# Optimization experiments

Hardware: AMD Instinct MI355X
Metric: run time of the kernel (lower is better)

Reference implementation:

```python
import jax, jax.numpy as jnp
import numpy as np


def setup_inputs() -> dict:
    key = jax.random.key(0)
    k1, k2 = jax.random.split(key)
    B, Fin, N = 8, 64, 4096
    Fout, K = 64, 20
    x = jax.random.normal(k1, (B, Fin, N), dtype=jnp.float32)
    W = jax.random.normal(k2, (Fout, 2 * Fin), dtype=jnp.float32) * (1.0 / np.sqrt(2 * Fin))
    b = jnp.zeros((Fout,), dtype=jnp.float32)
    return {"x": x, "W": W, "b": b, "k": K}


def reference(x, W, b, k):
    # x: [B, Fin, N]; W: [Fout, 2Fin] (1x1 conv weight); b: [Fout]
    B, Fin, N = x.shape
    xt = jnp.swapaxes(x, 1, 2)                      # [B, N, Fin]
    sq = jnp.sum(xt * xt, axis=2)                   # [B, N]
    # pairwise squared distances: ||xi||^2 - 2 xi.xj + ||xj||^2
    dist = -2.0 * jnp.einsum('bnf,bmf->bnm', xt, xt) + sq[:, :, None] + sq[:, None, :]
    # ascending sort, drop self (index 0), keep k nearest neighbors
    idx = jnp.argsort(dist, axis=2)[:, :, 1:k + 1]  # [B, N, k] int
    # gather neighbor features per batch
    nbr = jax.vmap(lambda pts, i: pts[i])(xt, idx)  # [B, N, k, Fin]
    central = xt[:, :, None, :]                     # [B, N, 1, Fin]
    ee = jnp.concatenate(
        [jnp.broadcast_to(central, (B, N, k, Fin)), nbr - central], axis=-1
    )                                               # [B, N, k, 2Fin]
    # 1x1 conv == dense over channel dim, then bias, then max over k
    h = jnp.einsum('bnkf,of->bnko', ee, W) + b      # [B, N, k, Fout]
    out = jnp.max(h, axis=2)                        # [B, N, Fout]
    return jnp.swapaxes(out, 1, 2)                  # [B, Fout, N]
```

## Files before the change

### kernel.cpp

```cpp
#include <hip/hip_runtime.h>
#include <hip/hip_bf16.h>
#include <float.h>


#define BB 8
#define FF 64
#define NN 4096
#define KK 20
#define CAP 60
#define SS 2
#define PAD 0.3f

typedef unsigned short ushort_t;
typedef unsigned long long u64;
typedef __attribute__((ext_vector_type(8))) _Float16 half8;
typedef __attribute__((ext_vector_type(4))) float floatx4;
typedef __attribute__((ext_vector_type(2))) float floatx2;
typedef __attribute__((ext_vector_type(2))) unsigned short ushortx2;
typedef __attribute__((ext_vector_type(4))) unsigned int uintx4;

__device__ __forceinline__ size_t plidx16(int b, int n, int k) {
  return ((size_t)b * 256 + (n >> 4)) * 1024 + (size_t)(k >> 3) * 128 + (size_t)(n & 15) * 8 + (k & 7);
}

__global__ void __launch_bounds__(256) prep_kernel(
    const float* __restrict__ x, const float* __restrict__ W,
    float* __restrict__ sq, float* __restrict__ Q,
    ushort_t* __restrict__ ph, ushort_t* __restrict__ pm)
{
  __shared__ float xs[64][65];
  __shared__ float w2[64][65];
  int t = threadIdx.x;
  int b = blockIdx.x >> 6;
  int n0 = (blockIdx.x & 63) << 6;
  const float* xb = x + (size_t)b * FF * NN;

  int nl = t & 63, fq = t >> 6;
  #pragma unroll
  for (int i = 0; i < 16; ++i) {
    int f = fq + i * 4;
    xs[f][nl] = xb[(size_t)f * NN + n0 + nl];
  }
  #pragma unroll
  for (int i = 0; i < 16; ++i) {
    int id = i * 256 + t;
    int o = id >> 6, f = id & 63;
    w2[o][f] = W[o * 128 + 64 + f];
  }
  __syncthreads();

  if (t < 64) {
    float s = 0.f;
    #pragma unroll
    for (int f = 0; f < FF; ++f) { float v = xs[f][t]; s += v * v; }
    sq[b * NN + n0 + t] = s;
  }
  int o = t & 63, g = t >> 6;
  for (int i = 0; i < 16; ++i) {
    int r = g + i * 4;
    int n = n0 + r;
    float acc = 0.f;
    #pragma unroll
    for (int f = 0; f < FF; ++f) acc += w2[o][f] * xs[f][r];
    Q[((size_t)b * NN + n) * FF + o] = acc;

    float v = xs[o][r] * 1.41421356237309515f;
    _Float16 hh = (_Float16)v;
    float hf = (float)hh;
    _Float16 mm = (_Float16)((v - hf) * 4096.0f);
    size_t pb = plidx16(b, n, o);
    ph[pb] = __builtin_bit_cast(unsigned short, hh);
    pm[pb] = __builtin_bit_cast(unsigned short, mm);
  }
}

__device__ __forceinline__ void bitonic32f(float& v0, float& v1, int l15)
{
  #pragma unroll
  for (int k = 2; k <= 32; k <<= 1) {
    #pragma unroll
    for (int j = k >> 1; j >= 1; j >>= 1) {
      bool dirup = ((2 * l15) & k) == 0;
      if (j >= 2) {
        int lj = j >> 1;
        float p0 = __shfl_xor(v0, lj, 16);
        float p1 = __shfl_xor(v1, lj, 16);
        bool lower = (l15 & lj) == 0;
        bool keepmin = (dirup == lower);
        v0 = keepmin ? fminf(v0, p0) : fmaxf(v0, p0);
        v1 = keepmin ? fminf(v1, p1) : fmaxf(v1, p1);
      } else {
        float lo = fminf(v0, v1), hi = fmaxf(v0, v1);
        v0 = dirup ? lo : hi;
        v1 = dirup ? hi : lo;
      }
    }
  }
}

__device__ __forceinline__ void bitonic64k(u64& v0, u64& v1, int l31)
{
  #pragma unroll
  for (int k = 2; k <= 64; k <<= 1) {
    #pragma unroll
    for (int j = k >> 1; j >= 1; j >>= 1) {
      bool dirup = ((2 * l31) & k) == 0;
      if (j >= 2) {
        int lj = j >> 1;
        u64 p0 = __shfl_xor(v0, lj, 32);
        u64 p1 = __shfl_xor(v1, lj, 32);
        bool lower = (l31 & lj) == 0;
        bool keepmin = (dirup == lower);
        u64 a0 = v0 < p0 ? v0 : p0, b0 = v0 < p0 ? p0 : v0;
        u64 a1 = v1 < p1 ? v1 : p1, b1 = v1 < p1 ? p1 : v1;
        v0 = keepmin ? a0 : b0;
        v1 = keepmin ? a1 : b1;
      } else {
        u64 lo = v0 < v1 ? v0 : v1, hi = v0 < v1 ? v1 : v0;
        v0 = dirup ? lo : hi;
        v1 = dirup ? hi : lo;
      }
    }
  }
}

__device__ __forceinline__ u64 mkkey(float d, unsigned short idx)
{
  unsigned ub = __float_as_uint(d);
  unsigned mono = ub ^ (0x80000000u | (unsigned)((int)ub >> 31));
  return ((u64)mono << 16) | idx;
}

__global__ void __launch_bounds__(256) knn_kernel(
    const ushort_t* __restrict__ ph, const ushort_t* __restrict__ pm,
    const float* __restrict__ sq, u64* __restrict__ keys2)
{
  __shared__ ushort_t stg[2][2][2048];
  __shared__ float    bufd[4][16][CAP];
  __shared__ ushort_t bufi[4][16][CAP];
  __shared__ int scnt[4][16];

  const int t = threadIdx.x;
  const int lane = t & 63;
  const int l15 = lane & 15;
  const int q = lane >> 4;
  const int wv = t >> 6;
  const int blk = blockIdx.x;
  const int b = blk & 7;
  const int k2 = blk >> 3;
  const int slice = k2 & 1;
  const int g = k2 >> 1;
  const int n0w = (g * 4 + wv) * 16;

  const float* __restrict__ sqb = sq + (size_t)b * NN;
  const float MS = 2.44140625e-4f;
  const int laneoff = q * 128 + l15 * 8;

  const bool hasdiag = ((n0w >> 11) == slice);
  const int dmc = (n0w & 2047) >> 5;

  half8 Ah[2], Am[2];
  {
    size_t abase = ((size_t)b * 256 + (n0w >> 4)) * 1024 + laneoff;
    #pragma unroll
    for (int s = 0; s < 2; ++s) {
      Ah[s] = *(const half8*)(ph + abase + s * 512);
      Am[s] = *(const half8*)(pm + abase + s * 512);
      uintx4 uh = __builtin_bit_cast(uintx4, Ah[s]); uh ^= 0x80008000u;
      uintx4 um = __builtin_bit_cast(uintx4, Am[s]); um ^= 0x80008000u;
      Ah[s] = __builtin_bit_cast(half8, uh);
      Am[s] = __builtin_bit_cast(half8, um);
    }
  }

  const size_t slb = (size_t)b * 262144 + (size_t)slice * 131072;
  const uintx4* gph = (const uintx4*)(ph + slb) + t;
  const uintx4* gpm = (const uintx4*)(pm + slb) + t;

  float m1[4], m2[4];
  #pragma unroll
  for (int r = 0; r < 4; ++r) { m1[r] = FLT_MAX; m2[r] = FLT_MAX; }

  {
    uintx4 v0s = gph[0];
    *((uintx4*)stg[0][0] + t) = v0s;
    __syncthreads();

    const float* psq = sqb + slice * 2048 + l15;
    for (int mc = 0; mc < 64; ++mc) {
      const int cur = mc & 1;
      uintx4 nx;
      if (mc < 63) nx = gph[(mc + 1) * 256];
      float sv0 = psq[0];
      float sv1 = psq[16];
      floatx4 a1[2];
      #pragma unroll
      for (int e = 0; e < 4; ++e) { a1[0][e] = sv0; a1[1][e] = sv1; }
      const ushort_t* sp = stg[cur][0] + laneoff;
      #pragma unroll
      for (int ti = 0; ti < 2; ++ti) {
        #pragma unroll
        for (int s = 0; s < 2; ++s) {
          half8 Bh = *(const half8*)(sp + ti * 1024 + s * 512);
          a1[ti] = __builtin_amdgcn_mfma_f32_16x16x32_f16(Ah[s], Bh, a1[ti], 0, 0, 0);
        }
      }
      if (hasdiag && mc == dmc) {
        const int m0 = slice * 2048 + mc * 32;
        #pragma unroll
        for (int ti = 0; ti < 2; ++ti) {
          int mcol = m0 + 16 * ti + l15;
          #pragma unroll
          for (int r = 0; r < 4; ++r)
            if (mcol == n0w + 4 * q + r) a1[ti][r] = FLT_MAX;
        }
      }
      #pragma unroll
      for (int r = 0; r < 4; ++r) {
        float c = fminf(a1[0][r], a1[1][r]);
        m2[r] = __builtin_amdgcn_fmed3f(c, m1[r], m2[r]);
        m1[r] = fminf(m1[r], c);
      }
      if (mc < 63) *((uintx4*)stg[cur ^ 1][0] + t) = nx;
      __syncthreads();
      psq += 32;
    }
  }

  float taupad[4];
  #pragma unroll
  for (int r = 0; r < 4; ++r) {
    float v0 = m1[r], v1 = m2[r];
    bitonic32f(v0, v1, l15);
    taupad[r] = __shfl(v1, 9, 16) + PAD;
  }

  int cnt[4];
  #pragma unroll
  for (int r = 0; r < 4; ++r) cnt[r] = 0;

  {
    uintx4 vh0 = gph[0];
    uintx4 vm0 = gpm[0];
    *((uintx4*)stg[0][0] + t) = vh0;
    *((uintx4*)stg[0][1] + t) = vm0;
    __syncthreads();

    const float* psq = sqb + slice * 2048 + l15;
    for (int mc = 0; mc < 64; ++mc) {
      const int cur = mc & 1;
      uintx4 nh, nm;
      if (mc < 63) { nh = gph[(mc + 1) * 256]; nm = gpm[(mc + 1) * 256]; }
      float sv0 = psq[0];
      float sv1 = psq[16];
      floatx4 a1[2], a2[2];
      #pragma unroll
      for (int e = 0; e < 4; ++e) {
        a1[0][e] = sv0; a1[1][e] = sv1;
        a2[0][e] = 0.f; a2[1][e] = 0.f;
      }
      const ushort_t* sp0 = stg[cur][0] + laneoff;
      const ushort_t* sp1 = stg[cur][1] + laneoff;
      #pragma unroll
      for (int ti = 0; ti < 2; ++ti) {
        #pragma unroll
        for (int s = 0; s < 2; ++s) {
          half8 Bh = *(const half8*)(sp0 + ti * 1024 + s * 512);
          half8 Bm = *(const half8*)(sp1 + ti * 1024 + s * 512);
          a1[ti] = __builtin_amdgcn_mfma_f32_16x16x32_f16(Ah[s], Bh, a1[ti], 0, 0, 0);
          a2[ti] = __builtin_amdgcn_mfma_f32_16x16x32_f16(Am[s], Bh, a2[ti], 0, 0, 0);
          a2[ti] = __builtin_amdgcn_mfma_f32_16x16x32_f16(Ah[s], Bm, a2[ti], 0, 0, 0);
        }
      }
      #pragma unroll
      for (int ti = 0; ti < 2; ++ti)
        #pragma unroll
        for (int r = 0; r < 4; ++r)
          a1[ti][r] = __builtin_fmaf(MS, a2[ti][r], a1[ti][r]);
      const int m0 = slice * 2048 + mc * 32;
      if (hasdiag && mc == dmc) {
        #pragma unroll
        for (int ti = 0; ti < 2; ++ti) {
          int mcol = m0 + 16 * ti + l15;
          #pragma unroll
          for (int r = 0; r < 4; ++r)
            if (mcol == n0w + 4 * q + r) a1[ti][r] = FLT_MAX;
        }
      }
      #pragma unroll
      for (int ti = 0; ti < 2; ++ti) {
        int mcol = m0 + 16 * ti + l15;
        #pragma unroll
        for (int r = 0; r < 4; ++r) {
          bool ok = a1[ti][r] <= taupad[r];
          unsigned long long bal = __ballot(ok);
          if (bal) {
            unsigned mh = (unsigned)((bal >> (q * 16)) & 0xFFFFull);
            int pre = __popc(mh & ((1u << l15) - 1u));
            int slot = cnt[r] + pre;
            if (ok && slot < CAP) {
              bufd[wv][4 * q + r][slot] = a1[ti][r];
              bufi[wv][4 * q + r][slot] = (ushort_t)mcol;
            }
            cnt[r] += __popc(mh);
          }
        }
      }
      if (mc < 63) {
        *((uintx4*)stg[cur ^ 1][0] + t) = nh;
        *((uintx4*)stg[cur ^ 1][1] + t) = nm;
      }
      __syncthreads();
      psq += 32;
    }
  }

  if (l15 == 0) {
    #pragma unroll
    for (int r = 0; r < 4; ++r) scnt[wv][4 * q + r] = cnt[r];
  }
  __builtin_amdgcn_s_waitcnt(0);

  const int l31 = t & 31;
  const int hfw = (t >> 5) & 1;
  #pragma unroll
  for (int i = 0; i < 8; ++i) {
    int rloc = hfw * 8 + i;
    int c = scnt[wv][rloc];
    c = c < CAP ? c : CAP;
    u64 k0 = ~0ull, k1 = ~0ull;
    if (2 * l31 < c) {
      floatx2  dv = *(const floatx2*)&bufd[wv][rloc][2 * l31];
      ushortx2 iv = *(const ushortx2*)&bufi[wv][rloc][2 * l31];
      k0 = mkkey(dv[0], iv[0]);
      if (2 * l31 + 1 < c) k1 = mkkey(dv[1], iv[1]);
    }
    bitonic64k(k0, k1, l31);
    u64 a = __shfl(k0, l31 >> 1, 32);
    u64 b2 = __shfl(k1, l31 >> 1, 32);
    u64 kv = (l31 & 1) ? b2 : a;
    if (l31 < KK) {
      size_t rowg = ((size_t)b * NN + n0w + rloc) * SS + slice;
      keys2[rowg * KK + l31] = kv;
    }
  }
}

__global__ void __launch_bounds__(256) merge_kernel(
    const u64* __restrict__ keys2, int* __restrict__ idxOut)
{
  int row = blockIdx.x * 256 + threadIdx.x;
  if (row >= BB * NN) return;
  u64 h[SS]; int p[SS];
  #pragma unroll
  for (int s = 0; s < SS; ++s) {
    p[s] = 0;
    h[s] = keys2[((size_t)row * SS + s) * KK];
  }
  int* op = idxOut + (size_t)row * KK;
  #pragma unroll
  for (int q = 0; q < KK; ++q) {
    int bs = 0;
    u64 bv = h[0];
    #pragma unroll
    for (int s = 1; s < SS; ++s) { if (h[s] < bv) { bv = h[s]; bs = s; } }
    op[q] = (int)(bv & 0xFFFFull);
    p[bs]++;
    h[bs] = (p[bs] < KK) ? keys2[((size_t)row * SS + bs) * KK + p[bs]] : ~0ull;
  }
}

__global__ void __launch_bounds__(256) gather_kernel(
    const float* __restrict__ x, const float* __restrict__ W,
    const float* __restrict__ bias,
    const float* __restrict__ Q, const int* __restrict__ idxIn,
    float* __restrict__ out)
{
  __shared__ float xs[64][65];
  __shared__ float wp[64][65];
  __shared__ float ot[64][65];
  __shared__ float bs[64];
  int t = threadIdx.x;
  int b = blockIdx.x >> 6;
  int n0 = (blockIdx.x & 63) << 6;
  const float* xb = x + (size_t)b * FF * NN;

  int nl0 = t & 63, fq = t >> 6;
  #pragma unroll
  for (int i = 0; i < 16; ++i) {
    int f = fq + i * 4;
    xs[f][nl0] = xb[(size_t)f * NN + n0 + nl0];
  }
  #pragma unroll
  for (int i = 0; i < 16; ++i) {
    int id = i * 256 + t;
    int o = id >> 6, f = id & 63;
    wp[o][f] = W[o * 128 + f] - W[o * 128 + 64 + f];
  }
  if (t < 64) bs[t] = bias[t];
  __syncthreads();

  int o = t & 63, g = t >> 6;
  for (int i = 0; i < 16; ++i) {
    int nl = g + i * 4;
    int n = n0 + nl;
    float p = bs[o];
    #pragma unroll
    for (int f = 0; f < FF; ++f) p += wp[o][f] * xs[f][nl];
    const int* ip = idxIn + ((size_t)b * NN + n) * KK;
    float m = -FLT_MAX;
    #pragma unroll
    for (int j = 0; j < KK; ++j) {
      int nb = ip[j];
      m = fmaxf(m, Q[((size_t)b * NN + nb) * FF + o]);
    }
    ot[nl][o] = p + m;
  }
  __syncthreads();
  for (int i = 0; i < 16; ++i) {
    int o2 = g + i * 4;
    int nl = t & 63;
    out[((size_t)b * FF + o2) * NN + n0 + nl] = ot[nl][o2];
  }
}

extern "C" void kernel_launch(void* const* d_in, const int* in_sizes, int n_in,
                              void* d_out, int out_size, void* d_ws, size_t ws_size,
                              hipStream_t stream)
{
  const float* x    = (const float*)d_in[0];
  const float* W    = (const float*)d_in[1];
  const float* bias = (const float*)d_in[2];
  float* out = (float*)d_out;

  int*   idxb = (int*)d_ws;
  float* sq   = (float*)(idxb + (size_t)BB * NN * KK);
  float* Q    = sq + (size_t)BB * NN;
  ushort_t* ph = (ushort_t*)(Q + (size_t)BB * NN * FF);
  ushort_t* pm = ph + (size_t)BB * NN * FF;
  u64*   keys2 = (u64*)(pm + (size_t)BB * NN * FF);

  prep_kernel<<<BB * (NN / 64), 256, 0, stream>>>(x, W, sq, Q, ph, pm);
  knn_kernel<<<BB * 64 * SS, 256, 0, stream>>>(ph, pm, sq, keys2);
  merge_kernel<<<(BB * NN + 255) / 256, 256, 0, stream>>>(keys2, idxb);
  gather_kernel<<<BB * (NN / 64), 256, 0, stream>>>(x, W, bias, Q, idxb, out);
}
```

Before: 256.8 us.

## Process 32 query rows per wave in kNN kernel to reuse B tiles

Each wave now computes distances for two 16-row query tiles instead of one. Every staged candidate fragment loaded from LDS therefore feeds twice as many MFMAs, and the knn grid is halved. This cuts LDS reads and global staging traffic per query. In exchange, registers per thread rise (twice the accumulators, thresholds and counters) and there are fewer blocks to spread across CUs. The candidate buffer cap is trimmed from 60 to 56 so the doubled LDS buffers fit.

```diff
diff --git a/kernel.cpp b/kernel.cpp
--- a/kernel.cpp
+++ b/kernel.cpp
@@ -7,7 +7,7 @@
 #define FF 64
 #define NN 4096
 #define KK 20
-#define CAP 60
+#define CAP 56
 #define SS 2
 #define PAD 0.3f
 
@@ -136,9 +136,9 @@
     const float* __restrict__ sq, u64* __restrict__ keys2)
 {
   __shared__ ushort_t stg[2][2][2048];
-  __shared__ float    bufd[4][16][CAP];
-  __shared__ ushort_t bufi[4][16][CAP];
-  __shared__ int scnt[4][16];
+  __shared__ float    bufd[4][32][CAP];
+  __shared__ ushort_t bufi[4][32][CAP];
+  __shared__ int scnt[4][32];
 
   const int t = threadIdx.x;
   const int lane = t & 63;
@@ -150,7 +150,7 @@
   const int k2 = blk >> 3;
   const int slice = k2 & 1;
   const int g = k2 >> 1;
-  const int n0w = (g * 4 + wv) * 16;
+  const int n0w = (g * 4 + wv) * 32;
 
   const float* __restrict__ sqb = sq + (size_t)b * NN;
   const float MS = 2.44140625e-4f;
@@ -159,17 +159,18 @@
   const bool hasdiag = ((n0w >> 11) == slice);
   const int dmc = (n0w & 2047) >> 5;
 
-  half8 Ah[2], Am[2];
-  {
-    size_t abase = ((size_t)b * 256 + (n0w >> 4)) * 1024 + laneoff;
+  half8 Ah[2][2], Am[2][2];
+  #pragma unroll
+  for (int w = 0; w < 2; ++w) {
+    size_t abase = ((size_t)b * 256 + (n0w >> 4) + w) * 1024 + laneoff;
     #pragma unroll
     for (int s = 0; s < 2; ++s) {
-      Ah[s] = *(const half8*)(ph + abase + s * 512);
-      Am[s] = *(const half8*)(pm + abase + s * 512);
-      uintx4 uh = __builtin_bit_cast(uintx4, Ah[s]); uh ^= 0x80008000u;
-      uintx4 um = __builtin_bit_cast(uintx4, Am[s]); um ^= 0x80008000u;
-      Ah[s] = __builtin_bit_cast(half8, uh);
-      Am[s] = __builtin_bit_cast(half8, um);
+      Ah[w][s] = *(const half8*)(ph + abase + s * 512);
+      Am[w][s] = *(const half8*)(pm + abase + s * 512);
+      uintx4 uh = __builtin_bit_cast(uintx4, Ah[w][s]); uh ^= 0x80008000u;
+      uintx4 um = __builtin_bit_cast(uintx4, Am[w][s]); um ^= 0x80008000u;
+      Ah[w][s] = __builtin_bit_cast(half8, uh);
+      Am[w][s] = __builtin_bit_cast(half8, um);
     }
   }
 
@@ -177,9 +178,9 @@
   const uintx4* gph = (const uintx4*)(ph + slb) + t;
   const uintx4* gpm = (const uintx4*)(pm + slb) + t;
 
-  float m1[4], m2[4];
-  #pragma unroll
-  for (int r = 0; r < 4; ++r) { m1[r] = FLT_MAX; m2[r] = FLT_MAX; }
+  float m1[8], m2[8];
+  #pragma unroll
+  for (int r = 0; r < 8; ++r) { m1[r] = FLT_MAX; m2[r] = FLT_MAX; }
 
   {
     uintx4 v0s = gph[0];
@@ -193,51 +194,60 @@
       if (mc < 63) nx = gph[(mc + 1) * 256];
       float sv0 = psq[0];
       float sv1 = psq[16];
-      floatx4 a1[2];
-      #pragma unroll
-      for (int e = 0; e < 4; ++e) { a1[0][e] = sv0; a1[1][e] = sv1; }
       const ushort_t* sp = stg[cur][0] + laneoff;
-      #pragma unroll
-      for (int ti = 0; ti < 2; ++ti) {
-        #pragma unroll
-        for (int s = 0; s < 2; ++s) {
-          half8 Bh = *(const half8*)(sp + ti * 1024 + s * 512);
-          a1[ti] = __builtin_amdgcn_mfma_f32_16x16x32_f16(Ah[s], Bh, a1[ti], 0, 0, 0);
-        }
+      half8 B00 = *(const half8*)(sp);
+      half8 B01 = *(const half8*)(sp + 512);
+      half8 B10 = *(const half8*)(sp + 1024);
+      half8 B11 = *(const half8*)(sp + 1536);
+      floatx4 a[2][2];
+      #pragma unroll
+      for (int w = 0; w < 2; ++w)
+        #pragma unroll
+        for (int e = 0; e < 4; ++e) { a[w][0][e] = sv0; a[w][1][e] = sv1; }
+      #pragma unroll
+      for (int w = 0; w < 2; ++w) {
+        a[w][0] = __builtin_amdgcn_mfma_f32_16x16x32_f16(Ah[w][0], B00, a[w][0], 0, 0, 0);
+        a[w][0] = __builtin_amdgcn_mfma_f32_16x16x32_f16(Ah[w][1], B01, a[w][0], 0, 0, 0);
+        a[w][1] = __builtin_amdgcn_mfma_f32_16x16x32_f16(Ah[w][0], B10, a[w][1], 0, 0, 0);
+        a[w][1] = __builtin_amdgcn_mfma_f32_16x16x32_f16(Ah[w][1], B11, a[w][1], 0, 0, 0);
       }
       if (hasdiag && mc == dmc) {
         const int m0 = slice * 2048 + mc * 32;
         #pragma unroll
-        for (int ti = 0; ti < 2; ++ti) {
-          int mcol = m0 + 16 * ti + l15;
+        for (int w = 0; w < 2; ++w)
           #pragma unroll
-          for (int r = 0; r < 4; ++r)
-            if (mcol == n0w + 4 * q + r) a1[ti][r] = FLT_MAX;
+          for (int ti = 0; ti < 2; ++ti) {
+            int mcol = m0 + 16 * ti + l15;
+            #pragma unroll
+            for (int r = 0; r < 4; ++r)
+              if (mcol == n0w + 16 * w + 4 * q + r) a[w][ti][r] = FLT_MAX;
+          }
+      }
+      #pragma unroll
+      for (int w = 0; w < 2; ++w)
+        #pragma unroll
+        for (int r = 0; r < 4; ++r) {
+          float c = fminf(a[w][0][r], a[w][1][r]);
+          m2[w * 4 + r] = __builtin_amdgcn_fmed3f(c, m1[w * 4 + r], m2[w * 4 + r]);
+          m1[w * 4 + r] = fminf(m1[w * 4 + r], c);
         }
-      }
-      #pragma unroll
-      for (int r = 0; r < 4; ++r) {
-        float c = fminf(a1[0][r], a1[1][r]);
-        m2[r] = __builtin_amdgcn_fmed3f(c, m1[r], m2[r]);
-        m1[r] = fminf(m1[r], c);
-      }
       if (mc < 63) *((uintx4*)stg[cur ^ 1][0] + t) = nx;
       __syncthreads();
       psq += 32;
     }
   }
 
-  float taupad[4];
-  #pragma unroll
-  for (int r = 0; r < 4; ++r) {
+  float taupad[8];
+  #pragma unroll
+  for (int r = 0; r < 8; ++r) {
     float v0 = m1[r], v1 = m2[r];
     bitonic32f(v0, v1, l15);
     taupad[r] = __shfl(v1, 9, 16) + PAD;
   }
 
-  int cnt[4];
-  #pragma unroll
-  for (int r = 0; r < 4; ++r) cnt[r] = 0;
+  int cnt[8];
+  #pragma unroll
+  for (int r = 0; r < 8; ++r) cnt[r] = 0;
 
   {
     uintx4 vh0 = gph[0];
@@ -253,59 +263,79 @@
       if (mc < 63) { nh = gph[(mc + 1) * 256]; nm = gpm[(mc + 1) * 256]; }
       float sv0 = psq[0];
       float sv1 = psq[16];
-      floatx4 a1[2], a2[2];
-      #pragma unroll
-      for (int e = 0; e < 4; ++e) {
-        a1[0][e] = sv0; a1[1][e] = sv1;
-        a2[0][e] = 0.f; a2[1][e] = 0.f;
-      }
       const ushort_t* sp0 = stg[cur][0] + laneoff;
       const ushort_t* sp1 = stg[cur][1] + laneoff;
-      #pragma unroll
-      for (int ti = 0; ti < 2; ++ti) {
-        #pragma unroll
-        for (int s = 0; s < 2; ++s) {
-          half8 Bh = *(const half8*)(sp0 + ti * 1024 + s * 512);
-          half8 Bm = *(const half8*)(sp1 + ti * 1024 + s * 512);
-          a1[ti] = __builtin_amdgcn_mfma_f32_16x16x32_f16(Ah[s], Bh, a1[ti], 0, 0, 0);
-          a2[ti] = __builtin_amdgcn_mfma_f32_16x16x32_f16(Am[s], Bh, a2[ti], 0, 0, 0);
-          a2[ti] = __builtin_amdgcn_mfma_f32_16x16x32_f16(Ah[s], Bm, a2[ti], 0, 0, 0);
+      half8 H00 = *(const half8*)(sp0);
+      half8 H01 = *(const half8*)(sp0 + 512);
+      half8 H10 = *(const half8*)(sp0 + 1024);
+      half8 H11 = *(const half8*)(sp0 + 1536);
+      half8 M00 = *(const half8*)(sp1);
+      half8 M01 = *(const half8*)(sp1 + 512);
+      half8 M10 = *(const half8*)(sp1 + 1024);
+      half8 M11 = *(const half8*)(sp1 + 1536);
+      floatx4 a1[2][2], a2[2][2];
+      #pragma unroll
+      for (int w = 0; w < 2; ++w)
+        #pragma unroll
+        for (int e = 0; e < 4; ++e) {
+          a1[w][0][e] = sv0; a1[w][1][e] = sv1;
+          a2[w][0][e] = 0.f; a2[w][1][e] = 0.f;
         }
-      }
-      #pragma unroll
-      for (int ti = 0; ti < 2; ++ti)
-        #pragma unroll
-        for (int r = 0; r < 4; ++r)
-          a1[ti][r] = __builtin_fmaf(MS, a2[ti][r], a1[ti][r]);
+      #pragma unroll
+      for (int w = 0; w < 2; ++w) {
+        a1[w][0] = __builtin_amdgcn_mfma_f32_16x16x32_f16(Ah[w][0], H00, a1[w][0], 0, 0, 0);
+        a1[w][0] = __builtin_amdgcn_mfma_f32_16x16x32_f16(Ah[w][1], H01, a1[w][0], 0, 0, 0);
+        a2[w][0] = __builtin_amdgcn_mfma_f32_16x16x32_f16(Am[w][0], H00, a2[w][0], 0, 0, 0);
+        a2[w][0] = __builtin_amdgcn_mfma_f32_16x16x32_f16(Am[w][1], H01, a2[w][0], 0, 0, 0);
+        a2[w][0] = __builtin_amdgcn_mfma_f32_16x16x32_f16(Ah[w][0], M00, a2[w][0], 0, 0, 0);
+        a2[w][0] = __builtin_amdgcn_mfma_f32_16x16x32_f16(Ah[w][1], M01, a2[w][0], 0, 0, 0);
+        a1[w][1] = __builtin_amdgcn_mfma_f32_16x16x32_f16(Ah[w][0], H10, a1[w][1], 0, 0, 0);
+        a1[w][1] = __builtin_amdgcn_mfma_f32_16x16x32_f16(Ah[w][1], H11, a1[w][1], 0, 0, 0);
+        a2[w][1] = __builtin_amdgcn_mfma_f32_16x16x32_f16(Am[w][0], H10, a2[w][1], 0, 0, 0);
+        a2[w][1] = __builtin_amdgcn_mfma_f32_16x16x32_f16(Am[w][1], H11, a2[w][1], 0, 0, 0);
+        a2[w][1] = __builtin_amdgcn_mfma_f32_16x16x32_f16(Ah[w][0], M10, a2[w][1], 0, 0, 0);
+        a2[w][1] = __builtin_amdgcn_mfma_f32_16x16x32_f16(Ah[w][1], M11, a2[w][1], 0, 0, 0);
+      }
+      #pragma unroll
+      for (int w = 0; w < 2; ++w)
+        #pragma unroll
+        for (int ti = 0; ti < 2; ++ti)
+          #pragma unroll
+          for (int r = 0; r < 4; ++r)
+            a1[w][ti][r] = __builtin_fmaf(MS, a2[w][ti][r], a1[w][ti][r]);
       const int m0 = slice * 2048 + mc * 32;
       if (hasdiag && mc == dmc) {
+        #pragma unroll
+        for (int w = 0; w < 2; ++w)
+          #pragma unroll
+          for (int ti = 0; ti < 2; ++ti) {
+            int mcol = m0 + 16 * ti + l15;
+            #pragma unroll
+            for (int r = 0; r < 4; ++r)
+              if (mcol == n0w + 16 * w + 4 * q + r) a1[w][ti][r] = FLT_MAX;
+          }
+      }
+      #pragma unroll
+      for (int w = 0; w < 2; ++w)
         #pragma unroll
         for (int ti = 0; ti < 2; ++ti) {
           int mcol = m0 + 16 * ti + l15;
           #pragma unroll
-          for (int r = 0; r < 4; ++r)
-            if (mcol == n0w + 4 * q + r) a1[ti][r] = FLT_MAX;
-        }
-      }
-      #pragma unroll
-      for (int ti = 0; ti < 2; ++ti) {
-        int mcol = m0 + 16 * ti + l15;
-        #pragma unroll
-        for (int r = 0; r < 4; ++r) {
-          bool ok = a1[ti][r] <= taupad[r];
-          unsigned long long bal = __ballot(ok);
-          if (bal) {
-            unsigned mh = (unsigned)((bal >> (q * 16)) & 0xFFFFull);
-            int pre = __popc(mh & ((1u << l15) - 1u));
-            int slot = cnt[r] + pre;
-            if (ok && slot < CAP) {
-              bufd[wv][4 * q + r][slot] = a1[ti][r];
-              bufi[wv][4 * q + r][slot] = (ushort_t)mcol;
+          for (int r = 0; r < 4; ++r) {
+            bool ok = a1[w][ti][r] <= taupad[w * 4 + r];
+            unsigned long long bal = __ballot(ok);
+            if (bal) {
+              unsigned mh = (unsigned)((bal >> (q * 16)) & 0xFFFFull);
+              int pre = __popc(mh & ((1u << l15) - 1u));
+              int slot = cnt[w * 4 + r] + pre;
+              if (ok && slot < CAP) {
+                bufd[wv][16 * w + 4 * q + r][slot] = a1[w][ti][r];
+                bufi[wv][16 * w + 4 * q + r][slot] = (ushort_t)mcol;
+              }
+              cnt[w * 4 + r] += __popc(mh);
             }
-            cnt[r] += __popc(mh);
           }
         }
-      }
       if (mc < 63) {
         *((uintx4*)stg[cur ^ 1][0] + t) = nh;
         *((uintx4*)stg[cur ^ 1][1] + t) = nm;
@@ -317,15 +347,17 @@
 
   if (l15 == 0) {
     #pragma unroll
-    for (int r = 0; r < 4; ++r) scnt[wv][4 * q + r] = cnt[r];
+    for (int w = 0; w < 2; ++w)
+      #pragma unroll
+      for (int r = 0; r < 4; ++r) scnt[wv][16 * w + 4 * q + r] = cnt[w * 4 + r];
   }
   __builtin_amdgcn_s_waitcnt(0);
 
   const int l31 = t & 31;
   const int hfw = (t >> 5) & 1;
   #pragma unroll
-  for (int i = 0; i < 8; ++i) {
-    int rloc = hfw * 8 + i;
+  for (int i = 0; i < 16; ++i) {
+    int rloc = hfw * 16 + i;
     int c = scnt[wv][rloc];
     c = c < CAP ? c : CAP;
     u64 k0 = ~0ull, k1 = ~0ull;
@@ -441,7 +473,7 @@
   u64*   keys2 = (u64*)(pm + (size_t)BB * NN * FF);
 
   prep_kernel<<<BB * (NN / 64), 256, 0, stream>>>(x, W, sq, Q, ph, pm);
-  knn_kernel<<<BB * 64 * SS, 256, 0, stream>>>(ph, pm, sq, keys2);
+  knn_kernel<<<BB * 32 * SS, 256, 0, stream>>>(ph, pm, sq, keys2);
   merge_kernel<<<(BB * NN + 255) / 256, 256, 0, stream>>>(keys2, idxb);
   gather_kernel<<<BB * (NN / 64), 256, 0, stream>>>(x, W, bias, Q, idxb, out);
 }
```

Result: slower. 285.1 us (+11.0%).

## Fuse per-slice top-k merge into gather kernel via bitonic sort

Applied to the files above, without the earlier changes.

Removes the separate merge kernel and instead has each gather wavefront-half load both slices' 20 sorted keys, sort the 40 keys with the existing bitonic routine, and broadcast neighbor indices by shuffle. This drops one kernel launch and the idx write/read round trip through global memory. The gather tile shrinks from 64 to 32 points per block to double the grid. Each point's merge is now done redundantly by every wave computing it, adding shuffle and sort work inside the gather loop.

```diff
diff --git a/kernel.cpp b/kernel.cpp
--- a/kernel.cpp
+++ b/kernel.cpp
@@ -346,50 +346,28 @@
   }
 }
 
-__global__ void __launch_bounds__(256) merge_kernel(
-    const u64* __restrict__ keys2, int* __restrict__ idxOut)
-{
-  int row = blockIdx.x * 256 + threadIdx.x;
-  if (row >= BB * NN) return;
-  u64 h[SS]; int p[SS];
-  #pragma unroll
-  for (int s = 0; s < SS; ++s) {
-    p[s] = 0;
-    h[s] = keys2[((size_t)row * SS + s) * KK];
-  }
-  int* op = idxOut + (size_t)row * KK;
-  #pragma unroll
-  for (int q = 0; q < KK; ++q) {
-    int bs = 0;
-    u64 bv = h[0];
-    #pragma unroll
-    for (int s = 1; s < SS; ++s) { if (h[s] < bv) { bv = h[s]; bs = s; } }
-    op[q] = (int)(bv & 0xFFFFull);
-    p[bs]++;
-    h[bs] = (p[bs] < KK) ? keys2[((size_t)row * SS + bs) * KK + p[bs]] : ~0ull;
-  }
-}
-
 __global__ void __launch_bounds__(256) gather_kernel(
     const float* __restrict__ x, const float* __restrict__ W,
     const float* __restrict__ bias,
-    const float* __restrict__ Q, const int* __restrict__ idxIn,
+    const float* __restrict__ Q, const u64* __restrict__ keys2,
     float* __restrict__ out)
 {
-  __shared__ float xs[64][65];
+  __shared__ float xs[64][33];
   __shared__ float wp[64][65];
-  __shared__ float ot[64][65];
+  __shared__ float ot[32][65];
   __shared__ float bs[64];
   int t = threadIdx.x;
-  int b = blockIdx.x >> 6;
-  int n0 = (blockIdx.x & 63) << 6;
+  int b = blockIdx.x >> 7;
+  int n0 = (blockIdx.x & 127) << 5;
   const float* xb = x + (size_t)b * FF * NN;
 
-  int nl0 = t & 63, fq = t >> 6;
-  #pragma unroll
-  for (int i = 0; i < 16; ++i) {
-    int f = fq + i * 4;
-    xs[f][nl0] = xb[(size_t)f * NN + n0 + nl0];
+  {
+    int nl = t & 31, f0 = t >> 5;
+    #pragma unroll
+    for (int i = 0; i < 8; ++i) {
+      int f = f0 + i * 8;
+      xs[f][nl] = xb[(size_t)f * NN + n0 + nl];
+    }
   }
   #pragma unroll
   for (int i = 0; i < 16; ++i) {
@@ -400,26 +378,36 @@
   if (t < 64) bs[t] = bias[t];
   __syncthreads();
 
-  int o = t & 63, g = t >> 6;
-  for (int i = 0; i < 16; ++i) {
+  const int o = t & 63, g = t >> 6;
+  const int l31 = t & 31;
+  for (int i = 0; i < 8; ++i) {
     int nl = g + i * 4;
     int n = n0 + nl;
     float p = bs[o];
     #pragma unroll
     for (int f = 0; f < FF; ++f) p += wp[o][f] * xs[f][nl];
-    const int* ip = idxIn + ((size_t)b * NN + n) * KK;
+
+    size_t kbase = ((size_t)b * NN + n) * SS * KK;
+    u64 k0 = (l31 < KK) ? keys2[kbase + l31]      : ~0ull;
+    u64 k1 = (l31 < KK) ? keys2[kbase + KK + l31] : ~0ull;
+    bitonic64k(k0, k1, l31);
+    u64 a = __shfl(k0, l31 >> 1, 32);
+    u64 b2 = __shfl(k1, l31 >> 1, 32);
+    u64 kv = (l31 & 1) ? b2 : a;
+
     float m = -FLT_MAX;
     #pragma unroll
     for (int j = 0; j < KK; ++j) {
-      int nb = ip[j];
+      int nb = (int)(__shfl(kv, j, 32) & 0xFFFFull);
       m = fmaxf(m, Q[((size_t)b * NN + nb) * FF + o]);
     }
     ot[nl][o] = p + m;
   }
   __syncthreads();
-  for (int i = 0; i < 16; ++i) {
-    int o2 = g + i * 4;
-    int nl = t & 63;
+  #pragma unroll
+  for (int i = 0; i < 8; ++i) {
+    int id = i * 256 + t;
+    int o2 = id >> 5, nl = id & 31;
     out[((size_t)b * FF + o2) * NN + n0 + nl] = ot[nl][o2];
   }
 }
@@ -442,6 +430,5 @@
 
   prep_kernel<<<BB * (NN / 64), 256, 0, stream>>>(x, W, sq, Q, ph, pm);
   knn_kernel<<<BB * 64 * SS, 256, 0, stream>>>(ph, pm, sq, keys2);
-  merge_kernel<<<(BB * NN + 255) / 256, 256, 0, stream>>>(keys2, idxb);
-  gather_kernel<<<BB * (NN / 64), 256, 0, stream>>>(x, W, bias, Q, idxb, out);
-}
+  gather_kernel<<<BB * (NN / 32), 256, 0, stream>>>(x, W, bias, Q, keys2, out);
+}
```

After: 264.4 us. +3.0%, slower.
